# Kernel optimization log

Hardware: AMD Instinct MI355X
Metric: run time of the kernel (lower is better)

The kernel has to match this reference:

```python
import jax, jax.numpy as jnp
import numpy as np

PS = 4        # bkg_patch_size
PD = 1        # replicate pad
UFSTRIDE = 2  # patch-extraction stride
STRIDE = 1    # correlation stride
SCALE = 10.0  # softmax_scale


def pad_edge(x):
    return jnp.pad(x, ((0, 0), (0, 0), (PD, PD), (PD, PD)), mode='edge')


def unfold(x, ps, stride):
    # x: (B,C,H,W) -> (B, L, C, ps, ps), row-major over patch grid (matches F.unfold)
    B, C, H, W = x.shape
    oh = (H - ps) // stride + 1
    ow = (W - ps) // stride + 1
    ih = jnp.arange(oh)[:, None] * stride + jnp.arange(ps)[None, :]  # (oh, ps)
    iw = jnp.arange(ow)[:, None] * stride + jnp.arange(ps)[None, :]  # (ow, ps)
    p = x[:, :, ih][:, :, :, :, iw]            # (B,C,oh,ps,ow,ps)
    p = p.transpose(0, 2, 4, 1, 3, 5)          # (B,oh,ow,C,ps,ps)
    return p.reshape(B, oh * ow, C, ps, ps)


def diag3(x):
    # conv2d with 3x3 identity kernel, padding=1: out[i,j] = in[i-1,j-1]+in[i,j]+in[i+1,j+1]
    B, one, N, M = x.shape
    xp = jnp.pad(x, ((0, 0), (0, 0), (1, 1), (1, 1)))
    return xp[:, :, 0:N, 0:M] + xp[:, :, 1:N + 1, 1:M + 1] + xp[:, :, 2:N + 2, 2:M + 2]


def setup_inputs() -> dict:
    key = jax.random.key(0)
    k1, k2, k3 = jax.random.split(key, 3)
    B, C, H, W = 4, 64, 64, 64
    f = jax.random.normal(k1, (B, C, H, W), dtype=jnp.float32)
    b = jax.random.normal(k2, (B, C, H, W), dtype=jnp.float32)
    mask = (jax.random.uniform(k3, (B, 1, H, W)) < 0.25).astype(jnp.float32)
    return {"f": f, "b": b, "mask": mask}


def reference(f, b, mask):
    B, C, H, W = b.shape
    maskc = 1.0 - mask
    # --- get_conv_kernel: per-(batch,channel) L2-normalize b, extract patch kernels ---
    bn = b / jnp.sqrt(jnp.sum(b * b, axis=(2, 3), keepdims=True) + 1e-8)
    kernel = unfold(pad_edge(bn), PS, UFSTRIDE)                 # (B, L, C, ps, ps)
    mk = unfold(pad_edge(maskc), PS, UFSTRIDE)                  # (B, L, 1, ps, ps)
    mmk = jnp.mean(mk, axis=(2, 3, 4))[:, :, None, None]        # (B, L, 1, 1)
    L = kernel.shape[1]

    # --- batched grouped cross-correlation: conv f with per-sample patch kernels ---
    fpatch = unfold(pad_edge(f), PS, STRIDE)                    # (B, P, C, ps, ps)
    hs = (H + 2 * PD - PS) // STRIDE + 1
    ws = (W + 2 * PD - PS) // STRIDE + 1
    cos = jnp.einsum('bpcij,blcij->blp', fpatch, kernel)        # (B, L, P)
    cos = cos.reshape(B, L, hs, ws)

    # --- fuse: diagonal 3x3 convs along two axis pairings ---
    hb, wb = H // 2, W // 2
    cs = L
    c1 = diag3(cos.reshape(B, 1, cs, hs * ws))
    c1 = c1.reshape(B, 1, hb, wb, hs, ws).transpose(0, 1, 3, 2, 5, 4).reshape(B, 1, cs, hs * ws)
    c1 = diag3(c1)
    c1 = c1.reshape(B, 1, hb, wb, hs, ws).transpose(0, 1, 3, 2, 5, 4)
    cos = c1.reshape(B, cs, hs, ws)

    # --- irregular mask logic ---
    mp = unfold(pad_edge(maskc), PS, STRIDE)                    # (B, P, 1, ps, ps)
    mmp = jnp.mean(mp, axis=(2, 3, 4)).reshape(B, 1, hs, ws)    # (B, 1, hs, ws)
    mm = (mmk > mmp).astype(cos.dtype)                          # (B, L, hs, ws)
    ppp = (mmp > 0.5).astype(cos.dtype)
    mm = mm * ppp + (mmk == 1.0).astype(cos.dtype)
    mm = (mm > 0).astype(cos.dtype)

    cos = cos * mm
    return jax.nn.softmax(cos * SCALE, axis=1)
```

## Files before the change

kernel.cpp:

```cpp
#include <hip/hip_runtime.h>
#include <math.h>

#define NB 4
#define NC 64
#define NL 1024
#define NP 3969
#define PHW 63

typedef unsigned short ushort_t;
typedef __attribute__((ext_vector_type(8))) short short8;
typedef __attribute__((ext_vector_type(16))) float floatx16;

#define A_BSTRIDE 1048576
#define B_BSTRIDE 4194304

__global__ __launch_bounds__(256) void prep_kernel(const float* __restrict__ bsrc,
                                                   const float* __restrict__ mask,
                                                   float* __restrict__ invn,
                                                   float* __restrict__ mmk,
                                                   float* __restrict__ mmp,
                                                   ushort_t* __restrict__ Bhi,
                                                   ushort_t* __restrict__ Blo) {
    int blk = blockIdx.x;
    if (blk < 256) {
        const float* src = bsrc + (size_t)blk * 4096;
        float s = 0.f;
        for (int i = threadIdx.x; i < 4096; i += 256) { float v = src[i]; s += v * v; }
#pragma unroll
        for (int off = 32; off > 0; off >>= 1) s += __shfl_down(s, off, 64);
        __shared__ float part[4];
        if ((threadIdx.x & 63) == 0) part[threadIdx.x >> 6] = s;
        __syncthreads();
        if (threadIdx.x == 0) {
            float t = part[0] + part[1] + part[2] + part[3];
            invn[blk] = 1.0f / sqrtf(t + 1e-8f);
        }
    } else if (blk < 335) {
        int id = (blk - 256) * 256 + threadIdx.x;
        if (id < NB * NL) {
            int b = id >> 10, l = id & 1023;
            int lh = l >> 5, lw = l & 31;
            const float* m = mask + b * 4096;
            float s = 0.f;
#pragma unroll
            for (int i = 0; i < 4; ++i) {
                int r = min(max(2 * lh - 1 + i, 0), 63);
#pragma unroll
                for (int j = 0; j < 4; ++j) {
                    int c = min(max(2 * lw - 1 + j, 0), 63);
                    s += 1.0f - m[r * 64 + c];
                }
            }
            mmk[id] = s * (1.0f / 16.0f);
        } else {
            int id2 = id - NB * NL;
            if (id2 < NB * NP) {
                int b = id2 / NP, p = id2 - b * NP;
                int ph = p / PHW, pw = p - ph * PHW;
                const float* m = mask + b * 4096;
                float s = 0.f;
#pragma unroll
                for (int i = 0; i < 4; ++i) {
                    int r = min(max(ph - 1 + i, 0), 63);
#pragma unroll
                    for (int j = 0; j < 4; ++j) {
                        int c = min(max(pw - 1 + j, 0), 63);
                        s += 1.0f - m[r * 64 + c];
                    }
                }
                mmp[id2] = s * (1.0f / 16.0f);
            }
        }
    } else {
        int idx = (blk - 335) * 256 + threadIdx.x;
        int b = idx >> 15;
        int r = idx & 32767;
        int mat = r >> 14;
        int o = r & 16383;
        ushort_t* base = (mat ? Blo : Bhi) + (size_t)b * B_BSTRIDE + 124 * 32768;
        uint4 z = {0u, 0u, 0u, 0u};
        ((uint4*)base)[o] = z;
    }
}

__device__ inline void split_bf16(float v, ushort_t& hv, ushort_t& lv) {
    unsigned u = __float_as_uint(v);
    unsigned rr = u + 0x7FFFu + ((u >> 16) & 1u);
    hv = (ushort_t)(rr >> 16);
    float fh = __uint_as_float(((unsigned)hv) << 16);
    float remv = v - fh;
    unsigned u2 = __float_as_uint(remv);
    unsigned rr2 = u2 + 0x7FFFu + ((u2 >> 16) & 1u);
    lv = (ushort_t)(rr2 >> 16);
}

__device__ inline int frag_addr(int row, int kc) {
    return ((row >> 5) * 64 + kc) * 512 + (row & 31) * 8;
}

__global__ __launch_bounds__(256) void split_kernel(const float* __restrict__ bsrc,
                                                    const float* __restrict__ invn,
                                                    ushort_t* __restrict__ Ahi,
                                                    ushort_t* __restrict__ Alo,
                                                    const float* __restrict__ fsrc,
                                                    ushort_t* __restrict__ Bhi,
                                                    ushort_t* __restrict__ Blo) {
    __shared__ float fl[32 * 257];
    int x = blockIdx.x, b = blockIdx.y, chalf = blockIdx.z;
    int t = threadIdx.x;
    if (x < 32) {
        int lh = x;
#pragma unroll
        for (int q = 0; q < 32; ++q) {
            int idx = t + (q << 8);
            int cl = idx >> 8, rem = idx & 255;
            int i = rem >> 6, s = rem & 63;
            int c = (chalf << 5) + cl;
            int r = min(max(2 * lh - 1 + i, 0), 63);
            fl[cl * 257 + rem] = bsrc[(((size_t)((b << 6) + c)) << 12) + (r << 6) + s];
        }
        __syncthreads();
        ushort_t* Ah = Ahi + (size_t)b * A_BSTRIDE;
        ushort_t* Al = Alo + (size_t)b * A_BSTRIDE;
#pragma unroll
        for (int q = 0; q < 4; ++q) {
            int pair = t + (q << 8);
            int lw = pair & 31, cl = pair >> 5;
            int c = (chalf << 5) + cl;
            float scale = invn[(b << 6) + c];
            const float* row = fl + cl * 257;
            __align__(16) ushort_t h[16];
            __align__(16) ushort_t lo[16];
#pragma unroll
            for (int i = 0; i < 4; ++i)
#pragma unroll
                for (int j = 0; j < 4; ++j) {
                    int s = min(max(2 * lw - 1 + j, 0), 63);
                    split_bf16(row[i * 64 + s] * scale, h[i * 4 + j], lo[i * 4 + j]);
                }
            int a = (lh * 64 + c) * 512 + lw * 8;
            *(uint4*)(Ah + a)       = *(uint4*)h;
            *(uint4*)(Ah + a + 256) = *(uint4*)(h + 8);
            *(uint4*)(Al + a)       = *(uint4*)lo;
            *(uint4*)(Al + a + 256) = *(uint4*)(lo + 8);
        }
    } else {
        int ph = x - 32;
#pragma unroll
        for (int q = 0; q < 32; ++q) {
            int idx = t + (q << 8);
            int cl = idx >> 8, rem = idx & 255;
            int i = rem >> 6, s = rem & 63;
            int c = (chalf << 5) + cl;
            int r = min(max(ph - 1 + i, 0), 63);
            fl[cl * 257 + rem] = fsrc[(((size_t)((b << 6) + c)) << 12) + (r << 6) + s];
        }
        __syncthreads();
        ushort_t* Bh = Bhi + (size_t)b * B_BSTRIDE;
        ushort_t* Bl = Blo + (size_t)b * B_BSTRIDE;
#pragma unroll
        for (int q = 0; q < 8; ++q) {
            int pair = t + (q << 8);
            int pw = pair & 63, cl = pair >> 6;
            if (pw < PHW) {
                int c = (chalf << 5) + cl;
                const float* row = fl + cl * 257;
                __align__(16) ushort_t h[16];
                __align__(16) ushort_t lo[16];
#pragma unroll
                for (int i = 0; i < 4; ++i)
#pragma unroll
                    for (int j = 0; j < 4; ++j) {
                        int s = min(max(pw - 1 + j, 0), 63);
                        split_bf16(row[i * 64 + s], h[i * 4 + j], lo[i * 4 + j]);
                    }
                int p = ph * PHW + pw;
                int a = frag_addr(p, c);
                *(uint4*)(Bh + a)       = *(uint4*)h;
                *(uint4*)(Bh + a + 256) = *(uint4*)(h + 8);
                *(uint4*)(Bl + a)       = *(uint4*)lo;
                *(uint4*)(Bl + a + 256) = *(uint4*)(lo + 8);
            }
        }
    }
}

__global__ __launch_bounds__(256, 2) void gemm_kernel(
    const ushort_t* __restrict__ Ahi, const ushort_t* __restrict__ Alo,
    const ushort_t* __restrict__ Bhi, const ushort_t* __restrict__ Blo,
    float* __restrict__ Rt) {
    __shared__ ushort_t smem[2][8][512];
    int tid = threadIdx.x;
    int lane = tid & 63, w = tid >> 6;
    int bid = blockIdx.x;
    int wid = ((bid & 7) << 6) + (bid >> 3);
    int b = wid >> 7;
    int rem = wid & 127;
    int lg = rem >> 4;
    int pg = rem & 15;
    int L0 = lg << 7, P0 = pg << 8;

    const ushort_t* asrc[2];
#pragma unroll
    for (int i = 0; i < 2; ++i) {
        int s = 2 * w + i;
        const ushort_t* base = ((s >> 2) ? Alo : Ahi) + (size_t)b * A_BSTRIDE;
        asrc[i] = base + (size_t)((L0 >> 5) + (s & 3)) * 32768 + (size_t)(lane << 3);
    }
    ushort_t* dst0 = &smem[0][2 * w][0];
    ushort_t* dst1 = &smem[1][2 * w][0];

    const ushort_t* bsrc[4];
#pragma unroll
    for (int i = 0; i < 4; ++i) {
        const ushort_t* base = ((i >> 1) ? Blo : Bhi) + (size_t)b * B_BSTRIDE;
        bsrc[i] = base + (size_t)((P0 >> 5) + 2 * w + (i & 1)) * 32768 + (size_t)(lane << 3);
    }

#define STAGEA(dstp, kc)                                                                   \
    do {                                                                                   \
        _Pragma("unroll")                                                                  \
        for (int i = 0; i < 2; ++i)                                                        \
            __builtin_amdgcn_global_load_lds(                                              \
                (const __attribute__((address_space(1))) void*)(asrc[i] + (size_t)(kc) * 512), \
                (__attribute__((address_space(3))) void*)((dstp) + i * 512),               \
                16, 0, 0);                                                                 \
    } while (0)

#define LOADB(dst, kc)                                                    \
    do {                                                                  \
        _Pragma("unroll")                                                 \
        for (int i = 0; i < 4; ++i)                                       \
            dst[i] = *(const short8*)(bsrc[i] + (size_t)(kc) * 512);      \
    } while (0)

#define COMP(bufi, bf)                                                                     \
    do {                                                                                   \
        short8 ahf[4], alf[4];                                                             \
        _Pragma("unroll")                                                                  \
        for (int lt = 0; lt < 4; ++lt) {                                                   \
            ahf[lt] = *(const short8*)(&smem[bufi][lt][lane << 3]);                        \
            alf[lt] = *(const short8*)(&smem[bufi][4 + lt][lane << 3]);                    \
        }                                                                                  \
        __builtin_amdgcn_s_setprio(1);                                                     \
        _Pragma("unroll")                                                                  \
        for (int pt = 0; pt < 2; ++pt)                                                     \
            _Pragma("unroll")                                                              \
            for (int lt = 0; lt < 4; ++lt)                                                 \
                acc[pt][lt] = __builtin_amdgcn_mfma_f32_32x32x16_bf16(bf[pt], ahf[lt], acc[pt][lt], 0, 0, 0); \
        _Pragma("unroll")                                                                  \
        for (int pt = 0; pt < 2; ++pt)                                                     \
            _Pragma("unroll")                                                              \
            for (int lt = 0; lt < 4; ++lt)                                                 \
                acc[pt][lt] = __builtin_amdgcn_mfma_f32_32x32x16_bf16(bf[pt], alf[lt], acc[pt][lt], 0, 0, 0); \
        _Pragma("unroll")                                                                  \
        for (int pt = 0; pt < 2; ++pt)                                                     \
            _Pragma("unroll")                                                              \
            for (int lt = 0; lt < 4; ++lt)                                                 \
                acc[pt][lt] = __builtin_amdgcn_mfma_f32_32x32x16_bf16(bf[2 + pt], ahf[lt], acc[pt][lt], 0, 0, 0); \
        __builtin_amdgcn_s_setprio(0);                                                     \
    } while (0)

    floatx16 acc[2][4];
#pragma unroll
    for (int i = 0; i < 2; ++i)
#pragma unroll
        for (int j = 0; j < 4; ++j)
#pragma unroll
            for (int r = 0; r < 16; ++r) acc[i][j][r] = 0.f;

    short8 bB0[4], bB1[4];
    LOADB(bB0, 0);
    STAGEA(dst0, 0);

    for (int t = 0; t < 64; t += 2) {
        LOADB(bB1, t + 1);
        STAGEA(dst1, t + 1);
        asm volatile("s_waitcnt vmcnt(6)" ::: "memory");
        __builtin_amdgcn_s_barrier();
        asm volatile("" ::: "memory");
        COMP(0, bB0);
        asm volatile("" ::: "memory");
        __builtin_amdgcn_s_barrier();
        if (t + 2 < 64) {
            LOADB(bB0, t + 2);
            STAGEA(dst0, t + 2);
            asm volatile("s_waitcnt vmcnt(6)" ::: "memory");
        } else {
            asm volatile("s_waitcnt vmcnt(0)" ::: "memory");
        }
        __builtin_amdgcn_s_barrier();
        asm volatile("" ::: "memory");
        COMP(1, bB1);
        asm volatile("" ::: "memory");
        __builtin_amdgcn_s_barrier();
    }
#undef STAGEA
#undef LOADB
#undef COMP

    int x = lane & 31, kg = lane >> 5;
    int pw0 = P0 + (w << 6);
#pragma unroll
    for (int pt = 0; pt < 2; ++pt)
#pragma unroll
        for (int lt = 0; lt < 4; ++lt)
#pragma unroll
            for (int r = 0; r < 16; ++r) {
                int p = pw0 + (pt << 5) + (r & 3) + ((r >> 2) << 3) + (kg << 2);
                int l = L0 + (lt << 5) + x;
                if (p < NP) Rt[((size_t)b * NP + p) * NL + l] = acc[pt][lt][r];
            }
}

__global__ __launch_bounds__(256) void softmax_fused_kernel(const float* __restrict__ Rt,
                                                            const float* __restrict__ mmkA,
                                                            const float* __restrict__ mmpA,
                                                            float* __restrict__ E) {
    __shared__ float ld0[1024], ld1[1024], ld2[1024];
    __shared__ float red[8];
    int p = blockIdx.x, b = blockIdx.y;
    int ph = p / PHW, pw = p - ph * PHW;
    int t = threadIdx.x;
    int lane = t & 63, w = t >> 6;
    int l0 = t << 2;

    bool okm = (p != 0), okp = (p != 3968);
    int Pm = (ph > 0) ? p - 63 : 3905 + pw;
    int Pp = (ph < 62) ? p + 63 : pw + 1;

    const float* Rb = Rt + (size_t)b * NP * NL;
#define BUILD(dst, q)                                                   \
    do {                                                                \
        const float* base = Rb + (size_t)(q) * NL;                      \
        float4 r = *(const float4*)(base + l0);                         \
        if ((q) > 0) {                                                  \
            const float* pm = base - NL;                                \
            r.x += (l0 > 0) ? pm[l0 - 1] : 0.f;                         \
            r.y += pm[l0];  r.z += pm[l0 + 1];  r.w += pm[l0 + 2];      \
        }                                                               \
        if ((q) < NP - 1) {                                             \
            const float* pp = base + NL;                                \
            r.x += pp[l0 + 1];  r.y += pp[l0 + 2];  r.z += pp[l0 + 3];  \
            r.w += (l0 + 4 < NL) ? pp[l0 + 4] : 0.f;                    \
        }                                                               \
        *(float4*)(dst + l0) = r;                                       \
    } while (0)

    BUILD(ld0, p);
    if (okm) BUILD(ld1, Pm);
    if (okp) BUILD(ld2, Pp);
#undef BUILD
    __syncthreads();

    float4 vc = *(const float4*)(ld0 + l0);
    float4 vm = {0.f, 0.f, 0.f, 0.f}, vp = {0.f, 0.f, 0.f, 0.f};
    if (okm) {
        if (l0 >= 32) vm = *(const float4*)(ld1 + l0 - 32);
        else {
            vm.x = (l0 == 0) ? 0.f : ld1[l0 + 991];
            vm.y = ld1[l0 + 992];
            vm.z = ld1[l0 + 993];
            vm.w = ld1[l0 + 994];
        }
    }
    if (okp) {
        if (l0 < 992) vp = *(const float4*)(ld2 + l0 + 32);
        else {
            vp.x = ld2[l0 - 991];
            vp.y = ld2[l0 - 990];
            vp.z = ld2[l0 - 989];
            vp.w = (l0 + 3 == 1023) ? 0.f : ld2[l0 - 988];
        }
    }
    float mmpv = mmpA[b * NP + p];
    float4 km = *(const float4*)(mmkA + b * NL + l0);
    float lg[4];
    float fsum[4] = {vc.x + vm.x + vp.x, vc.y + vm.y + vp.y,
                     vc.z + vm.z + vp.z, vc.w + vm.w + vp.w};
    float kk[4] = {km.x, km.y, km.z, km.w};
#pragma unroll
    for (int i = 0; i < 4; ++i) {
        float mmv = (((kk[i] > mmpv) && (mmpv > 0.5f)) || (kk[i] == 1.0f)) ? 1.0f : 0.0f;
        lg[i] = fsum[i] * mmv * 10.0f;
    }
    float mx = fmaxf(fmaxf(lg[0], lg[1]), fmaxf(lg[2], lg[3]));
#pragma unroll
    for (int off = 32; off >= 1; off >>= 1) mx = fmaxf(mx, __shfl_xor(mx, off, 64));
    if (lane == 0) red[w] = mx;
    __syncthreads();
    mx = fmaxf(fmaxf(red[0], red[1]), fmaxf(red[2], red[3]));
    float e[4];
    float s = 0.f;
#pragma unroll
    for (int i = 0; i < 4; ++i) { e[i] = expf(lg[i] - mx); s += e[i]; }
#pragma unroll
    for (int off = 32; off >= 1; off >>= 1) s += __shfl_xor(s, off, 64);
    if (lane == 0) red[4 + w] = s;
    __syncthreads();
    float rinv = 1.0f / (red[4] + red[5] + red[6] + red[7]);
    float4 ev = {e[0] * rinv, e[1] * rinv, e[2] * rinv, e[3] * rinv};
    *(float4*)(E + (((size_t)b * NP + p) << 10) + l0) = ev;
}

__global__ __launch_bounds__(256) void transpose_kernel(const float* __restrict__ E,
                                                        float* __restrict__ out) {
    __shared__ float tile[63 * 65];
    int pt = blockIdx.x;
    int lt = blockIdx.y;
    int b  = blockIdx.z;
    int t = threadIdx.x;
    int p0 = pt * 63, l0 = lt << 6;
    const float* Eb = E + ((size_t)b * NP << 10);
    {
        int j = t & 63, i4 = t >> 6;
#pragma unroll
        for (int k = 0; k < 16; ++k) {
            int i = (k << 2) + i4;
            if (i < 63) tile[i * 65 + j] = Eb[((size_t)(p0 + i) << 10) + l0 + j];
        }
    }
    __syncthreads();
    {
        int ii = t & 63, jj4 = t >> 6;
        if (ii < 63) {
#pragma unroll
            for (int k = 0; k < 16; ++k) {
                int jj = (k << 2) + jj4;
                out[((size_t)b * NL + l0 + jj) * NP + p0 + ii] = tile[ii * 65 + jj];
            }
        }
    }
}

extern "C" void kernel_launch(void* const* d_in, const int* in_sizes, int n_in,
                              void* d_out, int out_size, void* d_ws, size_t ws_size,
                              hipStream_t stream) {
    const float* f    = (const float*)d_in[0];
    const float* b    = (const float*)d_in[1];
    const float* mask = (const float*)d_in[2];
    float* out = (float*)d_out;

    float* Rt = (float*)d_out;

    float* wsf = (float*)d_ws;
    float* E  = wsf + 16257024;
    ushort_t* Ahi = (ushort_t*)d_ws;
    ushort_t* Alo = Ahi + (size_t)NB * A_BSTRIDE;
    ushort_t* Bhi = Alo + (size_t)NB * A_BSTRIDE;
    ushort_t* Blo = Bhi + (size_t)NB * B_BSTRIDE;
    float* invn = wsf + 32514048;
    float* mmk = invn + 256;
    float* mmp = mmk + 4096;

    prep_kernel<<<dim3(847), dim3(256), 0, stream>>>(b, mask, invn, mmk, mmp, Bhi, Blo);
    split_kernel<<<dim3(95, 4, 2), dim3(256), 0, stream>>>(b, invn, Ahi, Alo, f, Bhi, Blo);
    gemm_kernel<<<dim3(512), dim3(256), 0, stream>>>(Ahi, Alo, Bhi, Blo, Rt);
    softmax_fused_kernel<<<dim3(3969, 4), dim3(256), 0, stream>>>(Rt, mmk, mmp, E);
    transpose_kernel<<<dim3(63, 16, 4), dim3(256), 0, stream>>>(E, out);
}
```

Baseline: 263.2 us.

## Stage A tiles four k-chunks per barrier in GEMM main loop

The GEMM main loop now stages four K-chunks of the A operand into LDS per group instead of one, double-buffered across groups, with one barrier per group rather than two per chunk. The B fragments are still loaded from global per chunk into registers, ping-ponged between two register sets, with tuned vmcnt waits. The aim is to cut barrier and synchronization overhead while keeping loads overlapped with MFMA work. LDS usage per block grows fourfold (64 KB), which may reduce occupancy below the two blocks per CU requested, and the vmcnt counts must match the outstanding loads exactly.

```diff
diff --git a/kernel.cpp b/kernel.cpp
--- a/kernel.cpp
+++ b/kernel.cpp
@@ -189,7 +189,7 @@
     const ushort_t* __restrict__ Ahi, const ushort_t* __restrict__ Alo,
     const ushort_t* __restrict__ Bhi, const ushort_t* __restrict__ Blo,
     float* __restrict__ Rt) {
-    __shared__ ushort_t smem[2][8][512];
+    __shared__ ushort_t smem[2][4][8][512];
     int tid = threadIdx.x;
     int lane = tid & 63, w = tid >> 6;
     int bid = blockIdx.x;
@@ -207,8 +207,6 @@
         const ushort_t* base = ((s >> 2) ? Alo : Ahi) + (size_t)b * A_BSTRIDE;
         asrc[i] = base + (size_t)((L0 >> 5) + (s & 3)) * 32768 + (size_t)(lane << 3);
     }
-    ushort_t* dst0 = &smem[0][2 * w][0];
-    ushort_t* dst1 = &smem[1][2 * w][0];
 
     const ushort_t* bsrc[4];
 #pragma unroll
@@ -217,30 +215,33 @@
         bsrc[i] = base + (size_t)((P0 >> 5) + 2 * w + (i & 1)) * 32768 + (size_t)(lane << 3);
     }
 
-#define STAGEA(dstp, kc)                                                                   \
+#define STAGEA_G(bufi, g)                                                                  \
     do {                                                                                   \
         _Pragma("unroll")                                                                  \
-        for (int i = 0; i < 2; ++i)                                                        \
-            __builtin_amdgcn_global_load_lds(                                              \
-                (const __attribute__((address_space(1))) void*)(asrc[i] + (size_t)(kc) * 512), \
-                (__attribute__((address_space(3))) void*)((dstp) + i * 512),               \
-                16, 0, 0);                                                                 \
+        for (int c = 0; c < 4; ++c)                                                        \
+            _Pragma("unroll")                                                              \
+            for (int i = 0; i < 2; ++i)                                                    \
+                __builtin_amdgcn_global_load_lds(                                          \
+                    (const __attribute__((address_space(1))) void*)(asrc[i] + (size_t)(4 * (g) + c) * 512), \
+                    (__attribute__((address_space(3))) void*)(&smem[bufi][c][2 * w + i][0]), \
+                    16, 0, 0);                                                             \
     } while (0)
 
 #define LOADB(dst, kc)                                                    \
     do {                                                                  \
+        int kcc = min((kc), 63);                                          \
         _Pragma("unroll")                                                 \
         for (int i = 0; i < 4; ++i)                                       \
-            dst[i] = *(const short8*)(bsrc[i] + (size_t)(kc) * 512);      \
+            dst[i] = *(const short8*)(bsrc[i] + (size_t)kcc * 512);       \
     } while (0)
 
-#define COMP(bufi, bf)                                                                     \
+#define COMP(bufi, c, bf)                                                                  \
     do {                                                                                   \
         short8 ahf[4], alf[4];                                                             \
         _Pragma("unroll")                                                                  \
         for (int lt = 0; lt < 4; ++lt) {                                                   \
-            ahf[lt] = *(const short8*)(&smem[bufi][lt][lane << 3]);                        \
-            alf[lt] = *(const short8*)(&smem[bufi][4 + lt][lane << 3]);                    \
+            ahf[lt] = *(const short8*)(&smem[bufi][c][lt][lane << 3]);                     \
+            alf[lt] = *(const short8*)(&smem[bufi][c][4 + lt][lane << 3]);                 \
         }                                                                                  \
         __builtin_amdgcn_s_setprio(1);                                                     \
         _Pragma("unroll")                                                                  \
@@ -261,6 +262,9 @@
         __builtin_amdgcn_s_setprio(0);                                                     \
     } while (0)
 
+#define WAIT_B_MID()  asm volatile("s_waitcnt vmcnt(12)" ::: "memory")
+#define WAIT_B_LAST() asm volatile("s_waitcnt vmcnt(4)" ::: "memory")
+
     floatx16 acc[2][4];
 #pragma unroll
     for (int i = 0; i < 2; ++i)
@@ -269,35 +273,41 @@
 #pragma unroll
             for (int r = 0; r < 16; ++r) acc[i][j][r] = 0.f;
 
-    short8 bB0[4], bB1[4];
-    LOADB(bB0, 0);
-    STAGEA(dst0, 0);
-
-    for (int t = 0; t < 64; t += 2) {
-        LOADB(bB1, t + 1);
-        STAGEA(dst1, t + 1);
-        asm volatile("s_waitcnt vmcnt(6)" ::: "memory");
-        __builtin_amdgcn_s_barrier();
-        asm volatile("" ::: "memory");
-        COMP(0, bB0);
-        asm volatile("" ::: "memory");
-        __builtin_amdgcn_s_barrier();
-        if (t + 2 < 64) {
-            LOADB(bB0, t + 2);
-            STAGEA(dst0, t + 2);
-            asm volatile("s_waitcnt vmcnt(6)" ::: "memory");
-        } else {
-            asm volatile("s_waitcnt vmcnt(0)" ::: "memory");
-        }
-        __builtin_amdgcn_s_barrier();
-        asm volatile("" ::: "memory");
-        COMP(1, bB1);
-        asm volatile("" ::: "memory");
-        __builtin_amdgcn_s_barrier();
-    }
-#undef STAGEA
+    short8 bA[4], bBb[4];
+
+    STAGEA_G(0, 0);
+    LOADB(bA, 0);
+    asm volatile("s_waitcnt vmcnt(4)" ::: "memory");
+    __builtin_amdgcn_s_barrier();
+    asm volatile("" ::: "memory");
+
+    for (int g = 0; g < 16; ++g) {
+        int bufi = g & 1;
+        bool notlast = (g + 1 < 16);
+        if (notlast) STAGEA_G(bufi ^ 1, g + 1);
+        LOADB(bBb, 4 * g + 1);
+        if (notlast) WAIT_B_MID(); else WAIT_B_LAST();
+        COMP(bufi, 0, bA);
+        LOADB(bA, 4 * g + 2);
+        if (notlast) WAIT_B_MID(); else WAIT_B_LAST();
+        COMP(bufi, 1, bBb);
+        LOADB(bBb, 4 * g + 3);
+        if (notlast) WAIT_B_MID(); else WAIT_B_LAST();
+        COMP(bufi, 2, bA);
+        LOADB(bA, 4 * g + 4);
+        if (notlast) WAIT_B_MID(); else WAIT_B_LAST();
+        COMP(bufi, 3, bBb);
+        if (notlast) {
+            asm volatile("s_waitcnt vmcnt(4)" ::: "memory");
+            __builtin_amdgcn_s_barrier();
+            asm volatile("" ::: "memory");
+        }
+    }
+#undef STAGEA_G
 #undef LOADB
 #undef COMP
+#undef WAIT_B_MID
+#undef WAIT_B_LAST
 
     int x = lane & 31, kg = lane >> 5;
     int pw0 = P0 + (w << 6);
```

Result: no change. 263.1 us (-0.0%).
